# Performance work log

Hardware: AMD Instinct MI355X
Metric: run time of the kernel (lower is better)

## Reference

```python
import jax, jax.numpy as jnp
import numpy as np

OUT_F, IN_F, GROUP_SIZE = 4096, 4096, 64
N_GROUPS = OUT_F * IN_F // GROUP_SIZE  # 262144
B, S = 8, 2048


def setup_inputs() -> dict:
    key = jax.random.key(0)
    k1, k2, k3, k4, k5 = jax.random.split(key, 5)
    x = jax.random.normal(k1, (B, S, IN_F), dtype=jnp.float32)
    # packed 8-bit weights: '8bit_u8' packing is a plain uint8 store (values 0..255)
    W_q = jax.random.randint(k2, (GROUP_SIZE, N_GROUPS), 0, 256, dtype=jnp.int32)
    # per-group dequant params: scale = 1/quant_scale (small), zero = quant zero-point
    scale = jax.random.uniform(k3, (1, N_GROUPS), dtype=jnp.float32) * 0.01 + 1e-4
    zero = jax.random.uniform(k4, (1, N_GROUPS), dtype=jnp.float32) * 255.0
    bias = jax.random.normal(k5, (OUT_F,), dtype=jnp.float32)
    return {"x": x, "W_q": W_q, "scale": scale, "zero": zero, "bias": bias}


def reference(x, W_q, scale, zero, bias):
    # Quantizer.dequantize: unpack (identity for 8bit_u8), then ((W_q - zero) * scale).reshape(shape)
    W_r = ((W_q.astype(x.dtype) - zero) * scale).reshape(OUT_F, IN_F)  # [out, in]
    # forward_pytorch: F.linear(x, W_r, bias)
    return jnp.einsum("bsi,oi->bso", x, W_r) + bias
```

## Files before the change

kernel.cpp:

```cpp
#include <hip/hip_runtime.h>
#include <cstdio>
#include <cstdint>
#include <cstddef>

#define AS_GLOBAL __attribute__((address_space(1)))
#define AS_LDS    __attribute__((address_space(3)))

typedef __bf16 bf16x8 __attribute__((ext_vector_type(8)));
typedef float  f32x4  __attribute__((ext_vector_type(4)));

constexpr int OUT_F = 4096;
constexpr int IN_F  = 4096;
constexpr int MROWS = 8 * 2048;

__global__ void dequant_w(const int* __restrict__ Wq, const float* __restrict__ scale,
                          const float* __restrict__ zero, __bf16* __restrict__ Wb) {
    int t   = blockIdx.x * blockDim.x + threadIdx.x;
    int idx = t * 4;
    int o   = idx >> 12;
    int i   = idx & 4095;
    int n   = ((o & 63) << 12) | i;
    size_t flat = ((size_t)(o >> 6) << 18) + (size_t)n;
    int4   q = *(const int4*)(Wq + flat);
    float4 z = *(const float4*)(zero + n);
    float4 s = *(const float4*)(scale + n);
    __bf16 r[4];
    r[0] = (__bf16)(((float)q.x - z.x) * s.x);
    r[1] = (__bf16)(((float)q.y - z.y) * s.y);
    r[2] = (__bf16)(((float)q.z - z.z) * s.z);
    r[3] = (__bf16)(((float)q.w - z.w) * s.w);
    *(uint2*)(Wb + idx) = *(const uint2*)r;
}

__global__ void convert_x(const float* __restrict__ x, __bf16* __restrict__ xb) {
    size_t t   = (size_t)blockIdx.x * blockDim.x + threadIdx.x;
    size_t idx = t * 8;
    float4 a = *(const float4*)(x + idx);
    float4 b = *(const float4*)(x + idx + 4);
    __bf16 r[8];
    r[0] = (__bf16)a.x; r[1] = (__bf16)a.y; r[2] = (__bf16)a.z; r[3] = (__bf16)a.w;
    r[4] = (__bf16)b.x; r[5] = (__bf16)b.y; r[6] = (__bf16)b.z; r[7] = (__bf16)b.w;
    *(uint4*)(xb + idx) = *(const uint4*)r;
}

__device__ __forceinline__ void load16_to_lds(const void* g, void* lds) {
    __builtin_amdgcn_global_load_lds((AS_GLOBAL void*)g, (AS_LDS void*)lds, 16, 0, 0);
}

__global__ __launch_bounds__(512, 2) void gemm256(
    const __bf16* __restrict__ A,
    const __bf16* __restrict__ B,
    const float*  __restrict__ bias,
    float*        __restrict__ C)
{
    constexpr int K   = IN_F, N = OUT_F;
    constexpr int BK  = 32;
    constexpr int NT  = K / BK;
    constexpr int BUF = 32768;
    __shared__ __align__(16) char smem[4 * BUF];

    const int tid = threadIdx.x;
    const int l   = tid & 63;
    const int w   = tid >> 6;
    const int wr  = w >> 2;
    const int wc  = w & 3;

    const int bid = blockIdx.x;
    const int wg  = (bid & 7) * 128 + (bid >> 3);
    const int n0  = (wg & 15) * 256;
    const int m0  = (wg >> 4) * 256;

    const int srow   = l >> 2;
    const int schunk = (l & 3) ^ ((l >> 3) & 3);
    const __bf16* sA0 = A + (size_t)(m0 + (w*2+0)*16 + srow) * K + schunk*8;
    const __bf16* sA1 = A + (size_t)(m0 + (w*2+1)*16 + srow) * K + schunk*8;
    const __bf16* sB0 = B + (size_t)(n0 + (w*2+0)*16 + srow) * K + schunk*8;
    const __bf16* sB1 = B + (size_t)(n0 + (w*2+1)*16 + srow) * K + schunk*8;
    const int dstA0 = (w*2+0)*1024, dstA1 = (w*2+1)*1024;
    const int dstB0 = 16384 + dstA0, dstB1 = 16384 + dstA1;

    const int fr = l & 15, fg = l >> 4;
    const int in_off = fr*64 + ((fg ^ ((fr >> 1) & 3)) << 4);

    f32x4 acc[8][4] = {};

#define STAGE(t) do {                                                   \
        char* _b = smem + ((t) & 3) * BUF;                              \
        const int _k = (t) * BK;                                        \
        load16_to_lds(sA0 + _k, _b + dstA0);                            \
        load16_to_lds(sA1 + _k, _b + dstA1);                            \
        load16_to_lds(sB0 + _k, _b + dstB0);                            \
        load16_to_lds(sB1 + _k, _b + dstB1);                            \
    } while (0)

#define COMPUTE(t) do {                                                 \
        const char* _a  = smem + ((t) & 3) * BUF;                       \
        const char* _bb = _a + 16384;                                   \
        bf16x8 aF[8], bF[4];                                            \
        _Pragma("unroll")                                               \
        for (int mi = 0; mi < 8; ++mi)                                  \
            aF[mi] = *(const bf16x8*)(_a + (wr*8 + mi)*1024 + in_off);  \
        _Pragma("unroll")                                               \
        for (int ni = 0; ni < 4; ++ni)                                  \
            bF[ni] = *(const bf16x8*)(_bb + (wc*4 + ni)*1024 + in_off); \
        __builtin_amdgcn_s_setprio(1);                                  \
        _Pragma("unroll")                                               \
        for (int mi = 0; mi < 8; ++mi)                                  \
            _Pragma("unroll")                                           \
            for (int ni = 0; ni < 4; ++ni)                              \
                acc[mi][ni] = __builtin_amdgcn_mfma_f32_16x16x32_bf16(  \
                    aF[mi], bF[ni], acc[mi][ni], 0, 0, 0);              \
        __builtin_amdgcn_s_setprio(0);                                  \
    } while (0)

    STAGE(0); STAGE(1); STAGE(2);
    asm volatile("s_waitcnt vmcnt(8)" ::: "memory");
    asm volatile("s_barrier" ::: "memory");

#pragma unroll 4
    for (int T = 0; T < NT - 4; ++T) {
        STAGE(T + 3);
        COMPUTE(T);
        asm volatile("s_waitcnt vmcnt(8)" ::: "memory");
        asm volatile("s_barrier" ::: "memory");
    }
    STAGE(NT - 1);
    COMPUTE(NT - 4);
    asm volatile("s_waitcnt vmcnt(8)" ::: "memory");
    asm volatile("s_barrier" ::: "memory");
    COMPUTE(NT - 3);
    asm volatile("s_waitcnt vmcnt(4)" ::: "memory");
    asm volatile("s_barrier" ::: "memory");
    COMPUTE(NT - 2);
    asm volatile("s_waitcnt vmcnt(0)" ::: "memory");
    asm volatile("s_barrier" ::: "memory");
    COMPUTE(NT - 1);

#undef STAGE
#undef COMPUTE

    const int rb = (l >> 4) * 4;
    const int cl = l & 15;
#pragma unroll
    for (int ni = 0; ni < 4; ++ni) {
        const int   c  = n0 + wc * 64 + ni * 16 + cl;
        const float bv = bias[c];
#pragma unroll
        for (int mi = 0; mi < 8; ++mi) {
            const size_t base = (size_t)(m0 + wr * 128 + mi * 16 + rb) * N + c;
#pragma unroll
            for (int rg = 0; rg < 4; ++rg)
                C[base + (size_t)rg * N] = acc[mi][ni][rg] + bv;
        }
    }
}

extern "C" void kernel_launch(void* const* d_in, const int* in_sizes, int n_in,
                              void* d_out, int out_size, void* d_ws, size_t ws_size,
                              hipStream_t stream) {
    const float* x     = (const float*)d_in[0];
    const int*   Wq    = (const int*)d_in[1];
    const float* scale = (const float*)d_in[2];
    const float* zero  = (const float*)d_in[3];
    const float* bias  = (const float*)d_in[4];
    float* out = (float*)d_out;

    const size_t wbytes = (size_t)OUT_F * IN_F * 2;
    const size_t xbytes = (size_t)MROWS * IN_F * 2;
    if (ws_size < wbytes + xbytes) {
        fprintf(stderr, "kernel_launch: ws_size=%zu < needed %zu — aborting\n",
                ws_size, wbytes + xbytes);
        return;
    }
    __bf16* Wb = (__bf16*)d_ws;
    __bf16* xb = (__bf16*)((char*)d_ws + wbytes);

    dequant_w<<<(OUT_F * IN_F / 4) / 256, 256, 0, stream>>>(Wq, scale, zero, Wb);
    convert_x<<<((size_t)MROWS * IN_F / 8) / 256, 256, 0, stream>>>(x, xb);

    gemm256<<<dim3((MROWS / 256) * (OUT_F / 256)), dim3(512), 0, stream>>>(
        xb, Wb, bias, out);
}
```

Measured before the change: 937.3 us.

## Split GEMM main loop into half-tile phases interleaving LDS reads, loads and MFMA

Restructures the pipelined GEMM loop so each K-slice runs as two half phases. Each phase reads the A fragments plus two B fragments, issues half of the next stage's global-to-LDS loads, and runs 16 MFMAs, with explicit lgkmcnt waits and extra barriers in between. The goal is finer interleaving of memory traffic with matrix math and fewer live B registers. The cost is twice as many barriers per slice, and the hand-unrolled ring-buffer schedule has to keep the slot indices and wait counts correct.

```diff
diff --git a/kernel.cpp b/kernel.cpp
--- a/kernel.cpp
+++ b/kernel.cpp
@@ -47,6 +47,12 @@
     __builtin_amdgcn_global_load_lds((AS_GLOBAL void*)g, (AS_LDS void*)lds, 16, 0, 0);
 }
 
+#define BAR   asm volatile("s_barrier" ::: "memory")
+#define LGKM0 asm volatile("s_waitcnt lgkmcnt(0)" ::: "memory")
+#define VM8   asm volatile("s_waitcnt vmcnt(8)" ::: "memory")
+#define VM4   asm volatile("s_waitcnt vmcnt(4)" ::: "memory")
+#define VMDRAIN asm volatile("s_waitcnt vmcnt(0)" ::: "memory")
+
 __global__ __launch_bounds__(512, 2) void gemm256(
     const __bf16* __restrict__ A,
     const __bf16* __restrict__ B,
@@ -54,10 +60,8 @@
     float*        __restrict__ C)
 {
     constexpr int K   = IN_F, N = OUT_F;
-    constexpr int BK  = 32;
-    constexpr int NT  = K / BK;
-    constexpr int BUF = 32768;
-    __shared__ __align__(16) char smem[4 * BUF];
+    constexpr int NT  = K / 64;
+    __shared__ __align__(16) char smem[131072];
 
     const int tid = threadIdx.x;
     const int l   = tid & 63;
@@ -83,61 +87,67 @@
     const int in_off = fr*64 + ((fg ^ ((fr >> 1) & 3)) << 4);
 
     f32x4 acc[8][4] = {};
+    bf16x8 aF[8], bF[2];
 
-#define STAGE(t) do {                                                   \
-        char* _b = smem + ((t) & 3) * BUF;                              \
-        const int _k = (t) * BK;                                        \
-        load16_to_lds(sA0 + _k, _b + dstA0);                            \
-        load16_to_lds(sA1 + _k, _b + dstA1);                            \
-        load16_to_lds(sB0 + _k, _b + dstB0);                            \
-        load16_to_lds(sB1 + _k, _b + dstB1);                            \
-    } while (0)
+#define READ_A(sl) do { _Pragma("unroll")                                     \
+    for (int mi = 0; mi < 8; ++mi)                                            \
+        aF[mi] = *(const bf16x8*)(smem + (sl)*32768 + (wr*8 + mi)*1024 + in_off); } while (0)
 
-#define COMPUTE(t) do {                                                 \
-        const char* _a  = smem + ((t) & 3) * BUF;                       \
-        const char* _bb = _a + 16384;                                   \
-        bf16x8 aF[8], bF[4];                                            \
-        _Pragma("unroll")                                               \
-        for (int mi = 0; mi < 8; ++mi)                                  \
-            aF[mi] = *(const bf16x8*)(_a + (wr*8 + mi)*1024 + in_off);  \
-        _Pragma("unroll")                                               \
-        for (int ni = 0; ni < 4; ++ni)                                  \
-            bF[ni] = *(const bf16x8*)(_bb + (wc*4 + ni)*1024 + in_off); \
-        __builtin_amdgcn_s_setprio(1);                                  \
-        _Pragma("unroll")                                               \
-        for (int mi = 0; mi < 8; ++mi)                                  \
-            _Pragma("unroll")                                           \
-            for (int ni = 0; ni < 4; ++ni)                              \
-                acc[mi][ni] = __builtin_amdgcn_mfma_f32_16x16x32_bf16(  \
-                    aF[mi], bF[ni], acc[mi][ni], 0, 0, 0);              \
-        __builtin_amdgcn_s_setprio(0);                                  \
-    } while (0)
+#define READ_B(sl, nb) do {                                                   \
+    bF[0] = *(const bf16x8*)(smem + (sl)*32768 + 16384 + (wc*4 + (nb)    )*1024 + in_off); \
+    bF[1] = *(const bf16x8*)(smem + (sl)*32768 + 16384 + (wc*4 + (nb) + 1)*1024 + in_off); } while (0)
 
-    STAGE(0); STAGE(1); STAGE(2);
-    asm volatile("s_waitcnt vmcnt(8)" ::: "memory");
-    asm volatile("s_barrier" ::: "memory");
+#define STAGE_A(sl, koff) do {                                                \
+    load16_to_lds(sA0 + (koff), smem + (sl)*32768 + dstA0);                   \
+    load16_to_lds(sA1 + (koff), smem + (sl)*32768 + dstA1); } while (0)
 
-#pragma unroll 4
-    for (int T = 0; T < NT - 4; ++T) {
-        STAGE(T + 3);
-        COMPUTE(T);
-        asm volatile("s_waitcnt vmcnt(8)" ::: "memory");
-        asm volatile("s_barrier" ::: "memory");
+#define STAGE_B(sl, koff) do {                                                \
+    load16_to_lds(sB0 + (koff), smem + (sl)*32768 + dstB0);                   \
+    load16_to_lds(sB1 + (koff), smem + (sl)*32768 + dstB1); } while (0)
+
+#define MFMA16(nb) do {                                                       \
+    __builtin_amdgcn_s_setprio(1);                                            \
+    _Pragma("unroll")                                                         \
+    for (int mi = 0; mi < 8; ++mi) {                                          \
+        acc[mi][(nb)  ] = __builtin_amdgcn_mfma_f32_16x16x32_bf16(aF[mi], bF[0], acc[mi][(nb)  ], 0, 0, 0); \
+        acc[mi][(nb)+1] = __builtin_amdgcn_mfma_f32_16x16x32_bf16(aF[mi], bF[1], acc[mi][(nb)+1], 0, 0, 0); } \
+    __builtin_amdgcn_s_setprio(0); } while (0)
+
+    STAGE_A(0, 0);  STAGE_B(0, 0);
+    STAGE_A(1, 32); STAGE_B(1, 32);
+    STAGE_A(2, 64); STAGE_B(2, 64);
+    VM8; BAR;
+
+    for (int T = 0; T < NT - 3; T += 2) {
+        const int kA = T * 64;
+        READ_A(0); READ_B(0, 0); STAGE_A(3, kA +  96); BAR; LGKM0; MFMA16(0); BAR;
+        READ_B(0, 2);            STAGE_B(3, kA +  96); BAR; LGKM0; MFMA16(2); VM8; BAR;
+        READ_A(1); READ_B(1, 0); STAGE_A(0, kA + 128); BAR; LGKM0; MFMA16(0); BAR;
+        READ_B(1, 2);            STAGE_B(0, kA + 128); BAR; LGKM0; MFMA16(2); VM8; BAR;
+        READ_A(2); READ_B(2, 0); STAGE_A(1, kA + 160); BAR; LGKM0; MFMA16(0); BAR;
+        READ_B(2, 2);            STAGE_B(1, kA + 160); BAR; LGKM0; MFMA16(2); VM8; BAR;
+        READ_A(3); READ_B(3, 0); STAGE_A(2, kA + 192); BAR; LGKM0; MFMA16(0); BAR;
+        READ_B(3, 2);            STAGE_B(2, kA + 192); BAR; LGKM0; MFMA16(2); VM8; BAR;
     }
-    STAGE(NT - 1);
-    COMPUTE(NT - 4);
-    asm volatile("s_waitcnt vmcnt(8)" ::: "memory");
-    asm volatile("s_barrier" ::: "memory");
-    COMPUTE(NT - 3);
-    asm volatile("s_waitcnt vmcnt(4)" ::: "memory");
-    asm volatile("s_barrier" ::: "memory");
-    COMPUTE(NT - 2);
-    asm volatile("s_waitcnt vmcnt(0)" ::: "memory");
-    asm volatile("s_barrier" ::: "memory");
-    COMPUTE(NT - 1);
+    {
+        const int kA = (NT - 2) * 64;
+        READ_A(0); READ_B(0, 0); STAGE_A(3, kA + 96); BAR; LGKM0; MFMA16(0); BAR;
+        READ_B(0, 2);            STAGE_B(3, kA + 96); BAR; LGKM0; MFMA16(2); VM8; BAR;
+        READ_A(1); READ_B(1, 0);                      BAR; LGKM0; MFMA16(0); BAR;
+        READ_B(1, 2);                                 BAR; LGKM0; MFMA16(2); VM4; BAR;
+    }
+    {
+        READ_A(2); READ_B(2, 0); BAR; LGKM0; MFMA16(0); BAR;
+        READ_B(2, 2);            BAR; LGKM0; MFMA16(2); VMDRAIN; BAR;
+        READ_A(3); READ_B(3, 0); BAR; LGKM0; MFMA16(0); BAR;
+        READ_B(3, 2);            LGKM0; MFMA16(2);
+    }
 
-#undef STAGE
-#undef COMPUTE
+#undef READ_A
+#undef READ_B
+#undef STAGE_A
+#undef STAGE_B
+#undef MFMA16
 
     const int rb = (l >> 4) * 4;
     const int cl = l & 15;
```

After: 928.1 us. No clear change (-1.0%).
